# Optimization experiments

Measured on AMD Instinct MI355X. Metric: run time of the kernel, lower is better.

## Reference

```python
import jax, jax.numpy as jnp
import numpy as np
import math

N_USER = 100000
N_GAME = 50000
E = 200000
D = 256          # in_dim == out_dim
H = 8            # num_heads
SCALE = math.sqrt(D // H)  # sqrt(head_dim) = sqrt(32)


def setup_inputs() -> dict:
    key = jax.random.key(0)
    keys = jax.random.split(key, 64)
    it = iter(range(64))
    def nk():
        return keys[next(it)]
    s = 1.0 / math.sqrt(D)
    inp = {}
    inp["x_user"] = jax.random.normal(nk(), (N_USER, D), dtype=jnp.float32)
    inp["x_game"] = jax.random.normal(nk(), (N_GAME, D), dtype=jnp.float32)
    # node-type projections (k/q/v/out) for user and game
    for nt in ("user", "game"):
        for p in ("k", "q", "v", "out"):
            inp[f"W{p}_{nt}"] = jax.random.normal(nk(), (D, D), dtype=jnp.float32) * s
            inp[f"b{p}_{nt}"] = jax.random.normal(nk(), (D,), dtype=jnp.float32) * 0.01
    # edge-type attention + message transforms
    for et in ("played", "rev"):
        inp[f"Wa_{et}"] = jax.random.normal(nk(), (D, H), dtype=jnp.float32) * s
        inp[f"ba_{et}"] = jax.random.normal(nk(), (H,), dtype=jnp.float32) * 0.01
        inp[f"Wm_{et}"] = jax.random.normal(nk(), (D, D), dtype=jnp.float32) * s
        inp[f"bm_{et}"] = jax.random.normal(nk(), (D,), dtype=jnp.float32) * 0.01
    # edge indices: played (user -> game), rev_played (game -> user)
    inp["ei_played_src"] = jax.random.randint(nk(), (E,), 0, N_USER, dtype=jnp.int32)
    inp["ei_played_dst"] = jax.random.randint(nk(), (E,), 0, N_GAME, dtype=jnp.int32)
    inp["ei_rev_src"] = jax.random.randint(nk(), (E,), 0, N_GAME, dtype=jnp.int32)
    inp["ei_rev_dst"] = jax.random.randint(nk(), (E,), 0, N_USER, dtype=jnp.int32)
    return inp


def _lin(x, W, b):
    return x @ W + b


def _edge_pass(k_src_all, q_dst_all, v_src_all, Wa, ba, Wm, bm, src, dst, n_dst):
    # gather per-edge K/Q/V                                   [E, D]
    k_src = k_src_all[src]
    q_dst = q_dst_all[dst]
    v_src = v_src_all[src]
    # attention score MLP over head dim                       [E, H]
    scores = ((k_src * q_dst) @ Wa + ba) / SCALE
    attn = jax.nn.softmax(scores, axis=-1)  # softmax over heads (as in source)
    # message MLP                                             [E, D]
    msgs = v_src @ Wm + bm
    weighted = msgs * attn.mean(axis=-1, keepdims=True)
    # scatter-add to destination nodes
    agg = jax.ops.segment_sum(weighted, dst, num_segments=n_dst)
    cnt = jax.ops.segment_sum(jnp.ones((dst.shape[0], 1), weighted.dtype), dst, num_segments=n_dst)
    return agg, cnt


def reference(x_user, x_game,
              Wk_user, bk_user, Wq_user, bq_user, Wv_user, bv_user, Wout_user, bout_user,
              Wk_game, bk_game, Wq_game, bq_game, Wv_game, bv_game, Wout_game, bout_game,
              Wa_played, ba_played, Wm_played, bm_played,
              Wa_rev, ba_rev, Wm_rev, bm_rev,
              ei_played_src, ei_played_dst, ei_rev_src, ei_rev_dst):
    # per-node-type K/Q/V projections
    k_u = _lin(x_user, Wk_user, bk_user)
    q_u = _lin(x_user, Wq_user, bq_user)
    v_u = _lin(x_user, Wv_user, bv_user)
    k_g = _lin(x_game, Wk_game, bk_game)
    q_g = _lin(x_game, Wq_game, bq_game)
    v_g = _lin(x_game, Wv_game, bv_game)

    # user --played--> game
    agg_game, cnt_game = _edge_pass(k_u, q_g, v_u, Wa_played, ba_played, Wm_played, bm_played,
                                    ei_played_src, ei_played_dst, N_GAME)
    # game --rev_played--> user
    agg_user, cnt_user = _edge_pass(k_g, q_u, v_g, Wa_rev, ba_rev, Wm_rev, bm_rev,
                                    ei_rev_src, ei_rev_dst, N_USER)

    def finish(agg, cnt, x, Wout, bout):
        normed = agg / jnp.maximum(cnt, 1.0)
        return jax.nn.relu(_lin(normed, Wout, bout) + x)

    out_user = finish(agg_user, cnt_user, x_user, Wout_user, bout_user)
    out_game = finish(agg_game, cnt_game, x_game, Wout_game, bout_game)
    # concatenate node types for a single output array [N_USER+N_GAME, D]
    return jnp.concatenate([out_user, out_game], axis=0)
```

## Files before the change

kernel.cpp:

```cpp
#include <hip/hip_runtime.h>
#include <cstddef>
#include <cstdint>


#define DD 256
#define SCAN_CHUNK 2048

typedef __attribute__((ext_vector_type(8))) short short8;
typedef __attribute__((ext_vector_type(4))) float floatx4;

__device__ __forceinline__ short f2bf(float f) {
    union { float f; unsigned u; } c;
    c.f = f;
    unsigned r = c.u + 0x7fffu + ((c.u >> 16) & 1u);
    return (short)(r >> 16);
}

__device__ __forceinline__ float bflo(unsigned u) {
    union { unsigned u; float f; } c;
    c.u = u << 16;
    return c.f;
}
__device__ __forceinline__ float bfhi(unsigned u) {
    union { unsigned u; float f; } c;
    c.u = u & 0xffff0000u;
    return c.f;
}

__global__ __launch_bounds__(256) void fuseA(const float* __restrict__ A0,
                                             const float* __restrict__ B0,
                                             float* __restrict__ C0,
                                             const float* __restrict__ A1,
                                             const float* __restrict__ B1,
                                             float* __restrict__ C1,
                                             const int* __restrict__ dst0,
                                             int* __restrict__ cnt0, int E0,
                                             const int* __restrict__ dst1,
                                             int* __restrict__ cnt1, int E1) {
    __shared__ float As[DD];
    const int bid = blockIdx.x;
    const int c = threadIdx.x;
    if (bid < 512) {
        const int which = bid >> 8;
        const int r = bid & 255;
        const float* A = which ? A1 : A0;
        const float* B = which ? B1 : B0;
        float* C = which ? C1 : C0;
        As[c] = A[r * DD + c];
        __syncthreads();
        float acc = 0.f;
#pragma unroll 8
        for (int k = 0; k < DD; ++k) acc += As[k] * B[k * DD + c];
        C[r * DD + c] = acc;
    } else {
        const int nb0 = (E0 + 255) >> 8;
        const int b = bid - 512;
        if (b < nb0) {
            const int i = b * 256 + c;
            if (i < E0) atomicAdd(&cnt0[dst0[i]], 1);
        } else {
            const int i = (b - nb0) * 256 + c;
            if (i < E1) atomicAdd(&cnt1[dst1[i]], 1);
        }
    }
}

__global__ __launch_bounds__(256) void fuseB(const float* __restrict__ A0,
                                             const float* __restrict__ B0,
                                             short* __restrict__ C0,
                                             const float* __restrict__ A1,
                                             const float* __restrict__ B1,
                                             short* __restrict__ C1,
                                             int* __restrict__ off_g,
                                             int* __restrict__ sums_g, int n_g,
                                             int* __restrict__ off_u,
                                             int* __restrict__ sums_u, int n_u) {
    __shared__ float As[DD];
    __shared__ int ls[256];
    const int bid = blockIdx.x;
    const int tid = threadIdx.x;
    if (bid < 512) {
        const int which = bid >> 8;
        const int r = bid & 255;
        const int c = tid;
        const float* A = which ? A1 : A0;
        const float* B = which ? B1 : B0;
        short* C = which ? C1 : C0;
        As[c] = A[r * DD + c];
        __syncthreads();
        float acc = 0.f;
#pragma unroll 8
        for (int k = 0; k < DD; ++k) acc += As[k] * B[k * DD + c];
        const int idx = ((((r >> 5) * 16 + (c >> 4)) * 64 +
                          ((c & 15) | (((r >> 3) & 3) << 4))) << 3) + (r & 7);
        C[idx] = f2bf(acc * 0.125f);
    } else {
        const int nch_g = (n_g + SCAN_CHUNK - 1) / SCAN_CHUNK;
        const int b = bid - 512;
        int* off;
        int* sums;
        int n, cb;
        if (b < nch_g) { off = off_g; sums = sums_g; n = n_g; cb = b; }
        else { off = off_u; sums = sums_u; n = n_u; cb = b - nch_g; }
        const int base = cb * SCAN_CHUNK + tid * 8;
        int v[8];
        int s = 0;
#pragma unroll
        for (int i = 0; i < 8; ++i) {
            const int idx = base + i;
            v[i] = (idx < n) ? off[idx] : 0;
            s += v[i];
        }
        ls[tid] = s;
        __syncthreads();
        for (int d = 1; d < 256; d <<= 1) {
            const int t = (tid >= d) ? ls[tid - d] : 0;
            __syncthreads();
            ls[tid] += t;
            __syncthreads();
        }
        int excl = tid ? ls[tid - 1] : 0;
        if (tid == 255) sums[cb] = ls[255];
#pragma unroll
        for (int i = 0; i < 8; ++i) {
            const int idx = base + i;
            if (idx < n) off[idx] = excl;
            excl += v[i];
        }
    }
}

__global__ __launch_bounds__(256) void fuseC(const float* __restrict__ bv0,
                                             const float* __restrict__ Wm0,
                                             const float* __restrict__ bm0,
                                             const float* __restrict__ Wout0,
                                             float* __restrict__ bb0,
                                             const float* __restrict__ bv1,
                                             const float* __restrict__ Wm1,
                                             const float* __restrict__ bm1,
                                             const float* __restrict__ Wout1,
                                             float* __restrict__ bb1,
                                             int* __restrict__ sums_g, int nch_g,
                                             int* __restrict__ sums_u, int nch_u) {
    __shared__ float t[DD];
    __shared__ int ls[256];
    const int tid = threadIdx.x;
    if (blockIdx.x < 2) {
        const int w = blockIdx.x;
        const float* bv = w ? bv1 : bv0;
        const float* Wm = w ? Wm1 : Wm0;
        const float* bm = w ? bm1 : bm0;
        const float* Wout = w ? Wout1 : Wout0;
        float* bb = w ? bb1 : bb0;
        float acc = bm[tid];
#pragma unroll 8
        for (int k = 0; k < DD; ++k) acc += bv[k] * Wm[k * DD + tid];
        t[tid] = acc;
        __syncthreads();
        float acc2 = 0.f;
#pragma unroll 8
        for (int k = 0; k < DD; ++k) acc2 += t[k] * Wout[k * DD + tid];
        bb[tid] = acc2 * 0.125f;
    } else {
        int* sums = (blockIdx.x == 2) ? sums_g : sums_u;
        const int nch = (blockIdx.x == 2) ? nch_g : nch_u;
        ls[tid] = (tid < nch) ? sums[tid] : 0;
        __syncthreads();
        for (int d = 1; d < 256; d <<= 1) {
            const int t2 = (tid >= d) ? ls[tid - d] : 0;
            __syncthreads();
            ls[tid] += t2;
            __syncthreads();
        }
        if (tid < nch) sums[tid] = tid ? ls[tid - 1] : 0;
    }
}

__global__ __launch_bounds__(256) void fuseD(int* __restrict__ off_g,
                                             const int* __restrict__ sums_g,
                                             int* __restrict__ cur_g, int n_g, int Eg,
                                             int* __restrict__ off_u,
                                             const int* __restrict__ sums_u,
                                             int* __restrict__ cur_u, int n_u, int Eu) {
    const int gidx = blockIdx.x * 256 + threadIdx.x;
    const int span_g = n_g + 1;
    if (gidx < span_g) {
        if (gidx < n_g) {
            const int v = off_g[gidx] + sums_g[gidx / SCAN_CHUNK];
            off_g[gidx] = v;
            cur_g[gidx] = v;
        } else {
            off_g[n_g] = Eg;
        }
    } else {
        const int idx = gidx - span_g;
        if (idx < n_u) {
            const int v = off_u[idx] + sums_u[idx / SCAN_CHUNK];
            off_u[idx] = v;
            cur_u[idx] = v;
        } else if (idx == n_u) {
            off_u[n_u] = Eu;
        }
    }
}

__global__ __launch_bounds__(256, 4) void fuseE(
    const int* __restrict__ src0, const int* __restrict__ dst0,
    int* __restrict__ cur0, int* __restrict__ perm0, int E0,
    const int* __restrict__ src1, const int* __restrict__ dst1,
    int* __restrict__ cur1, int* __restrict__ perm1, int E1,
    const float* __restrict__ x_user, const float* __restrict__ x_game,
    const short* __restrict__ Bswp, const short* __restrict__ Bswr,
    short* __restrict__ Yp, short* __restrict__ Yr,
    int n_user, int n_game, int nyb_u, int nyb_g) {
    __shared__ short As[32][264];
    const int bid = blockIdx.x;
    const int tid = threadIdx.x;
    const int nyb = nyb_u + nyb_g;
    if (bid < nyb) {
        const int wave = __builtin_amdgcn_readfirstlane(tid >> 6);
        const int lane = tid & 63;
        const float* X;
        short* Y;
        const short* Bsw;
        int M, r0;
        if (bid < nyb_u) { X = x_user; Y = Yp; Bsw = Bswp; M = n_user; r0 = bid * 32; }
        else { X = x_game; Y = Yr; Bsw = Bswr; M = n_game; r0 = (bid - nyb_u) * 32; }

#pragma unroll
        for (int j = 0; j < 8; ++j) {
            const int lr = wave * 8 + j;
            const int r = r0 + lr;
            short4 b4 = {0, 0, 0, 0};
            if (r < M) {
                const float4 v = ((const float4*)(X + (size_t)r * DD))[lane];
                b4.x = f2bf(v.x);
                b4.y = f2bf(v.y);
                b4.z = f2bf(v.z);
                b4.w = f2bf(v.w);
            }
            *(short4*)&As[lr][lane * 4] = b4;
        }
        __syncthreads();

        const int quad = lane >> 4;
        const int l16 = lane & 15;
        floatx4 cacc[2][4];
#pragma unroll
        for (int rt = 0; rt < 2; ++rt)
#pragma unroll
            for (int ct = 0; ct < 4; ++ct) cacc[rt][ct] = (floatx4){0.f, 0.f, 0.f, 0.f};

        for (int kb8 = 0; kb8 < 8; ++kb8) {
            short8 af[2];
#pragma unroll
            for (int rt = 0; rt < 2; ++rt)
                af[rt] = *(const short8*)&As[rt * 16 + l16][kb8 * 32 + quad * 8];
            short8 bf[4];
            const short* bp = Bsw + (((size_t)(kb8 * 16 + wave * 4) * 64 + lane) << 3);
#pragma unroll
            for (int ct = 0; ct < 4; ++ct)
                bf[ct] = *(const short8*)(bp + (ct << 9));
#pragma unroll
            for (int rt = 0; rt < 2; ++rt)
#pragma unroll
                for (int ct = 0; ct < 4; ++ct)
                    cacc[rt][ct] = __builtin_amdgcn_mfma_f32_16x16x32_bf16(
                        af[rt], bf[ct], cacc[rt][ct], 0, 0, 0);
        }
        __syncthreads();

#pragma unroll
        for (int rt = 0; rt < 2; ++rt)
#pragma unroll
            for (int ct = 0; ct < 4; ++ct)
#pragma unroll
                for (int j = 0; j < 4; ++j)
                    As[rt * 16 + quad * 4 + j][wave * 64 + ct * 16 + l16] =
                        f2bf(cacc[rt][ct][j]);
        __syncthreads();
#pragma unroll
        for (int j = 0; j < 8; ++j) {
            const int lr = wave * 8 + j;
            const int r = r0 + lr;
            if (r < M)
                *(short4*)(Y + (size_t)r * DD + lane * 4) =
                    *(const short4*)&As[lr][lane * 4];
        }
    } else {
        const int b = bid - nyb;
        const int nb0 = (E0 + 255) >> 8;
        if (b < nb0) {
            const int i = b * 256 + tid;
            if (i < E0) {
                const int pos = atomicAdd(&cur0[dst0[i]], 1);
                perm0[pos] = src0[i];
            }
        } else {
            const int i = (b - nb0) * 256 + tid;
            if (i < E1) {
                const int pos = atomicAdd(&cur1[dst1[i]], 1);
                perm1[pos] = src1[i];
            }
        }
    }
}

__global__ __launch_bounds__(256, 4) void agg_relu(
    const short* __restrict__ Yp, const short* __restrict__ Yr,
    const int* __restrict__ perm_rev, const int* __restrict__ off_user,
    const float* __restrict__ bb_rev, const float* __restrict__ bout_user,
    const int* __restrict__ perm_played, const int* __restrict__ off_game,
    const float* __restrict__ bb_played, const float* __restrict__ bout_game,
    const float* __restrict__ x_user, const float* __restrict__ x_game,
    float* __restrict__ outp, int n_user, int n_game, int nb_game) {
    const int tid = threadIdx.x;
    const int wave = __builtin_amdgcn_readfirstlane(tid >> 6);
    const int lane = tid & 63;
    const int n0 = lane * 4;

    const short* Y;
    const int* perm;
    const int* off;
    const float* bb;
    const float* bout;
    const float* x_res;
    float* out;
    int M, r0;
    if ((int)blockIdx.x < nb_game) {
        Y = Yp;
        perm = perm_played;
        off = off_game;
        bb = bb_played;
        bout = bout_game;
        x_res = x_game;
        out = outp + (size_t)n_user * DD;
        M = n_game;
        r0 = (int)blockIdx.x * 32;
    } else {
        Y = Yr;
        perm = perm_rev;
        off = off_user;
        bb = bb_rev;
        bout = bout_user;
        x_res = x_user;
        out = outp;
        M = n_user;
        r0 = ((int)blockIdx.x - nb_game) * 32;
    }

    int e[8], en[8], deg[8];
    float4 acc[8];
#pragma unroll
    for (int j = 0; j < 8; ++j) {
        const int r = r0 + wave * 8 + j;
        e[j] = (r < M) ? off[r] : 0;
        en[j] = (r < M) ? off[r + 1] : 0;
        deg[j] = en[j] - e[j];
        acc[j].x = 0.f;
        acc[j].y = 0.f;
        acc[j].z = 0.f;
        acc[j].w = 0.f;
    }
    int mdeg = 0;
#pragma unroll
    for (int j = 0; j < 8; ++j) mdeg = max(mdeg, deg[j]);

    for (int t = 0; t < mdeg; ++t) {
        uint2 d[8];
        bool h[8];
#pragma unroll
        for (int j = 0; j < 8; ++j) {
            h[j] = e[j] < en[j];
            if (h[j]) {
                const int s = perm[e[j]++];
                d[j] = *(const uint2*)(Y + (size_t)s * DD + n0);
            }
        }
#pragma unroll
        for (int j = 0; j < 8; ++j) {
            if (h[j]) {
                acc[j].x += bflo(d[j].x);
                acc[j].y += bfhi(d[j].x);
                acc[j].z += bflo(d[j].y);
                acc[j].w += bfhi(d[j].y);
            }
        }
    }

    const float4 bbv = *(const float4*)(bb + n0);
    const float4 bov = *(const float4*)(bout + n0);
#pragma unroll
    for (int j = 0; j < 8; ++j) {
        const int r = r0 + wave * 8 + j;
        if (r < M) {
            const float inv = 1.0f / fmaxf((float)deg[j], 1.0f);
            const float beta = (deg[j] > 0) ? 1.0f : 0.0f;
            const float4 xr = *(const float4*)(x_res + (size_t)r * DD + n0);
            float4 o;
            o.x = fmaxf(acc[j].x * inv + beta * bbv.x + bov.x + xr.x, 0.f);
            o.y = fmaxf(acc[j].y * inv + beta * bbv.y + bov.y + xr.y, 0.f);
            o.z = fmaxf(acc[j].z * inv + beta * bbv.z + bov.z + xr.z, 0.f);
            o.w = fmaxf(acc[j].w * inv + beta * bbv.w + bov.w + xr.w, 0.f);
            *(float4*)(out + (size_t)r * DD + n0) = o;
        }
    }
}

extern "C" void kernel_launch(void* const* d_in, const int* in_sizes, int n_in,
                              void* d_out, int out_size, void* d_ws, size_t ws_size,
                              hipStream_t stream) {
    const float* x_user = (const float*)d_in[0];
    const float* x_game = (const float*)d_in[1];
    const float* Wv_user = (const float*)d_in[6];
    const float* bv_user = (const float*)d_in[7];
    const float* Wout_user = (const float*)d_in[8];
    const float* bout_user = (const float*)d_in[9];
    const float* Wv_game = (const float*)d_in[14];
    const float* bv_game = (const float*)d_in[15];
    const float* Wout_game = (const float*)d_in[16];
    const float* bout_game = (const float*)d_in[17];
    const float* Wm_played = (const float*)d_in[20];
    const float* bm_played = (const float*)d_in[21];
    const float* Wm_rev = (const float*)d_in[24];
    const float* bm_rev = (const float*)d_in[25];
    const int* ei_played_src = (const int*)d_in[26];
    const int* ei_played_dst = (const int*)d_in[27];
    const int* ei_rev_src = (const int*)d_in[28];
    const int* ei_rev_dst = (const int*)d_in[29];

    const int n_user = in_sizes[0] / DD;
    const int n_game = in_sizes[1] / DD;
    const int e_played = in_sizes[26];
    const int e_rev = in_sizes[28];

    float* out = (float*)d_out;

    float* fws = (float*)d_ws;
    float* T0 = fws;
    float* T1 = T0 + DD * DD;
    float* bb_played = T1 + DD * DD;
    float* bb_rev = bb_played + DD;
    short* Bsw_played = (short*)(bb_rev + DD);
    short* Bsw_rev = Bsw_played + DD * DD;
    int* iws = (int*)(Bsw_rev + DD * DD);
    int* off_game = iws;
    int* off_user = off_game + (n_game + 1);
    int* cursor_game = off_user + (n_user + 1);
    int* cursor_user = cursor_game + n_game;
    int* sums_game = cursor_user + n_user;
    int* sums_user = sums_game + 256;
    int* perm_played = sums_user + 256;
    int* perm_rev = perm_played + e_played;
    uintptr_t yaddr = (uintptr_t)(perm_rev + e_rev);
    yaddr = (yaddr + 255) & ~(uintptr_t)255;
    short* Yp = (short*)yaddr;
    short* Yr = Yp + (size_t)n_user * DD;
    (void)ws_size; (void)n_in; (void)out_size;

    hipMemsetAsync(off_game, 0, (size_t)(n_game + n_user + 2) * sizeof(int), stream);

    const int nbh_p = (e_played + 255) / 256;
    const int nbh_r = (e_rev + 255) / 256;
    const int nch_g = (n_game + SCAN_CHUNK - 1) / SCAN_CHUNK;
    const int nch_u = (n_user + SCAN_CHUNK - 1) / SCAN_CHUNK;

    fuseA<<<512 + nbh_p + nbh_r, 256, 0, stream>>>(
        Wv_user, Wm_played, T0, Wv_game, Wm_rev, T1,
        ei_played_dst, off_game, e_played, ei_rev_dst, off_user, e_rev);
    fuseB<<<512 + nch_g + nch_u, 256, 0, stream>>>(
        T0, Wout_game, Bsw_played, T1, Wout_user, Bsw_rev,
        off_game, sums_game, n_game, off_user, sums_user, n_user);
    fuseC<<<4, 256, 0, stream>>>(
        bv_user, Wm_played, bm_played, Wout_game, bb_played,
        bv_game, Wm_rev, bm_rev, Wout_user, bb_rev,
        sums_game, nch_g, sums_user, nch_u);
    const int ntot = (n_game + 1) + (n_user + 1);
    fuseD<<<(ntot + 255) / 256, 256, 0, stream>>>(
        off_game, sums_game, cursor_game, n_game, e_played,
        off_user, sums_user, cursor_user, n_user, e_rev);
    const int nyb_u = (n_user + 31) / 32;
    const int nyb_g = (n_game + 31) / 32;
    fuseE<<<nyb_u + nyb_g + nbh_p + nbh_r, 256, 0, stream>>>(
        ei_played_src, ei_played_dst, cursor_game, perm_played, e_played,
        ei_rev_src, ei_rev_dst, cursor_user, perm_rev, e_rev,
        x_user, x_game, Bsw_played, Bsw_rev, Yp, Yr,
        n_user, n_game, nyb_u, nyb_g);

    const int nb_game = (n_game + 31) / 32;
    const int nb_user = (n_user + 31) / 32;
    agg_relu<<<nb_game + nb_user, 256, 0, stream>>>(
        Yp, Yr, perm_rev, off_user, bb_rev, bout_user,
        perm_played, off_game, bb_played, bout_game,
        x_user, x_game, out, n_user, n_game, nb_game);
}
```

Baseline: 486.6 us.

## Merge all stages into one persistent kernel with global barriers

Replaces six kernel launches with a single persistent kernel of 1024 blocks that moves between stages through atomic-counter grid barriers. The bf16 MFMA projection tiles are split across barrier phases so they run alongside the scan, cursor and permutation work, hiding the small serial stages. This removes launch gaps and tail effects, but the grid barriers need every block resident at once (deadlock risk otherwise), and the fixed split points ya/yb are tuned by hand.

```diff
diff --git a/kernel.cpp b/kernel.cpp
--- a/kernel.cpp
+++ b/kernel.cpp
@@ -5,6 +5,8 @@
 
 #define DD 256
 #define SCAN_CHUNK 2048
+#define NB 1024
+#define NT 256
 
 typedef __attribute__((ext_vector_type(8))) short short8;
 typedef __attribute__((ext_vector_type(4))) float floatx4;
@@ -15,7 +17,6 @@
     unsigned r = c.u + 0x7fffu + ((c.u >> 16) & 1u);
     return (short)(r >> 16);
 }
-
 __device__ __forceinline__ float bflo(unsigned u) {
     union { unsigned u; float f; } c;
     c.u = u << 16;
@@ -27,295 +28,106 @@
     return c.f;
 }
 
-__global__ __launch_bounds__(256) void fuseA(const float* __restrict__ A0,
-                                             const float* __restrict__ B0,
-                                             float* __restrict__ C0,
-                                             const float* __restrict__ A1,
-                                             const float* __restrict__ B1,
-                                             float* __restrict__ C1,
-                                             const int* __restrict__ dst0,
-                                             int* __restrict__ cnt0, int E0,
-                                             const int* __restrict__ dst1,
-                                             int* __restrict__ cnt1, int E1) {
-    __shared__ float As[DD];
-    const int bid = blockIdx.x;
-    const int c = threadIdx.x;
-    if (bid < 512) {
-        const int which = bid >> 8;
-        const int r = bid & 255;
-        const float* A = which ? A1 : A0;
-        const float* B = which ? B1 : B0;
-        float* C = which ? C1 : C0;
-        As[c] = A[r * DD + c];
-        __syncthreads();
-        float acc = 0.f;
-#pragma unroll 8
-        for (int k = 0; k < DD; ++k) acc += As[k] * B[k * DD + c];
-        C[r * DD + c] = acc;
-    } else {
-        const int nb0 = (E0 + 255) >> 8;
-        const int b = bid - 512;
-        if (b < nb0) {
-            const int i = b * 256 + c;
-            if (i < E0) atomicAdd(&cnt0[dst0[i]], 1);
-        } else {
-            const int i = (b - nb0) * 256 + c;
-            if (i < E1) atomicAdd(&cnt1[dst1[i]], 1);
-        }
-    }
-}
-
-__global__ __launch_bounds__(256) void fuseB(const float* __restrict__ A0,
-                                             const float* __restrict__ B0,
-                                             short* __restrict__ C0,
-                                             const float* __restrict__ A1,
-                                             const float* __restrict__ B1,
-                                             short* __restrict__ C1,
-                                             int* __restrict__ off_g,
-                                             int* __restrict__ sums_g, int n_g,
-                                             int* __restrict__ off_u,
-                                             int* __restrict__ sums_u, int n_u) {
-    __shared__ float As[DD];
-    __shared__ int ls[256];
-    const int bid = blockIdx.x;
+__device__ __forceinline__ void gbar(int* bar, int target) {
+    __syncthreads();
+    if (threadIdx.x == 0) {
+        __threadfence();
+        __hip_atomic_fetch_add(bar, 1, __ATOMIC_ACQ_REL, __HIP_MEMORY_SCOPE_AGENT);
+        while (__hip_atomic_load(bar, __ATOMIC_ACQUIRE, __HIP_MEMORY_SCOPE_AGENT) < target)
+            __builtin_amdgcn_s_sleep(8);
+        __threadfence();
+    }
+    __syncthreads();
+}
+
+__device__ void ytile(int t, char* smem_,
+                      const float* __restrict__ x_user, const float* __restrict__ x_game,
+                      const short* __restrict__ Bswp, const short* __restrict__ Bswr,
+                      short* __restrict__ Yp, short* __restrict__ Yr,
+                      int n_user, int n_game, int nyb_u) {
+    short (*As)[264] = (short(*)[264])smem_;
     const int tid = threadIdx.x;
-    if (bid < 512) {
-        const int which = bid >> 8;
-        const int r = bid & 255;
-        const int c = tid;
-        const float* A = which ? A1 : A0;
-        const float* B = which ? B1 : B0;
-        short* C = which ? C1 : C0;
-        As[c] = A[r * DD + c];
-        __syncthreads();
-        float acc = 0.f;
-#pragma unroll 8
-        for (int k = 0; k < DD; ++k) acc += As[k] * B[k * DD + c];
-        const int idx = ((((r >> 5) * 16 + (c >> 4)) * 64 +
-                          ((c & 15) | (((r >> 3) & 3) << 4))) << 3) + (r & 7);
-        C[idx] = f2bf(acc * 0.125f);
-    } else {
-        const int nch_g = (n_g + SCAN_CHUNK - 1) / SCAN_CHUNK;
-        const int b = bid - 512;
-        int* off;
-        int* sums;
-        int n, cb;
-        if (b < nch_g) { off = off_g; sums = sums_g; n = n_g; cb = b; }
-        else { off = off_u; sums = sums_u; n = n_u; cb = b - nch_g; }
-        const int base = cb * SCAN_CHUNK + tid * 8;
-        int v[8];
-        int s = 0;
-#pragma unroll
-        for (int i = 0; i < 8; ++i) {
-            const int idx = base + i;
-            v[i] = (idx < n) ? off[idx] : 0;
-            s += v[i];
-        }
-        ls[tid] = s;
-        __syncthreads();
-        for (int d = 1; d < 256; d <<= 1) {
-            const int t = (tid >= d) ? ls[tid - d] : 0;
-            __syncthreads();
-            ls[tid] += t;
-            __syncthreads();
-        }
-        int excl = tid ? ls[tid - 1] : 0;
-        if (tid == 255) sums[cb] = ls[255];
-#pragma unroll
-        for (int i = 0; i < 8; ++i) {
-            const int idx = base + i;
-            if (idx < n) off[idx] = excl;
-            excl += v[i];
-        }
-    }
-}
-
-__global__ __launch_bounds__(256) void fuseC(const float* __restrict__ bv0,
-                                             const float* __restrict__ Wm0,
-                                             const float* __restrict__ bm0,
-                                             const float* __restrict__ Wout0,
-                                             float* __restrict__ bb0,
-                                             const float* __restrict__ bv1,
-                                             const float* __restrict__ Wm1,
-                                             const float* __restrict__ bm1,
-                                             const float* __restrict__ Wout1,
-                                             float* __restrict__ bb1,
-                                             int* __restrict__ sums_g, int nch_g,
-                                             int* __restrict__ sums_u, int nch_u) {
-    __shared__ float t[DD];
-    __shared__ int ls[256];
+    const int wave = tid >> 6;
+    const int lane = tid & 63;
+    const float* X;
+    short* Y;
+    const short* Bsw;
+    int M, r0;
+    if (t < nyb_u) { X = x_user; Y = Yp; Bsw = Bswp; M = n_user; r0 = t * 32; }
+    else { X = x_game; Y = Yr; Bsw = Bswr; M = n_game; r0 = (t - nyb_u) * 32; }
+
+#pragma unroll
+    for (int j = 0; j < 8; ++j) {
+        const int lr = wave * 8 + j;
+        const int r = r0 + lr;
+        short4 b4 = {0, 0, 0, 0};
+        if (r < M) {
+            const float4 v = ((const float4*)(X + (size_t)r * DD))[lane];
+            b4.x = f2bf(v.x);
+            b4.y = f2bf(v.y);
+            b4.z = f2bf(v.z);
+            b4.w = f2bf(v.w);
+        }
+        *(short4*)&As[lr][lane * 4] = b4;
+    }
+    __syncthreads();
+
+    const int quad = lane >> 4;
+    const int l16 = lane & 15;
+    floatx4 cacc[2][4];
+#pragma unroll
+    for (int rt = 0; rt < 2; ++rt)
+#pragma unroll
+        for (int ct = 0; ct < 4; ++ct) cacc[rt][ct] = (floatx4){0.f, 0.f, 0.f, 0.f};
+
+    for (int kb8 = 0; kb8 < 8; ++kb8) {
+        short8 af[2];
+#pragma unroll
+        for (int rt = 0; rt < 2; ++rt)
+            af[rt] = *(const short8*)&As[rt * 16 + l16][kb8 * 32 + quad * 8];
+        short8 bf[4];
+        const short* bp = Bsw + (((size_t)(kb8 * 16 + wave * 4) * 64 + lane) << 3);
+#pragma unroll
+        for (int ct = 0; ct < 4; ++ct)
+            bf[ct] = *(const short8*)(bp + (ct << 9));
+#pragma unroll
+        for (int rt = 0; rt < 2; ++rt)
+#pragma unroll
+            for (int ct = 0; ct < 4; ++ct)
+                cacc[rt][ct] = __builtin_amdgcn_mfma_f32_16x16x32_bf16(
+                    af[rt], bf[ct], cacc[rt][ct], 0, 0, 0);
+    }
+    __syncthreads();
+
+#pragma unroll
+    for (int rt = 0; rt < 2; ++rt)
+#pragma unroll
+        for (int ct = 0; ct < 4; ++ct)
+#pragma unroll
+            for (int j = 0; j < 4; ++j)
+                As[rt * 16 + quad * 4 + j][wave * 64 + ct * 16 + l16] =
+                    f2bf(cacc[rt][ct][j]);
+    __syncthreads();
+#pragma unroll
+    for (int j = 0; j < 8; ++j) {
+        const int lr = wave * 8 + j;
+        const int r = r0 + lr;
+        if (r < M)
+            *(short4*)(Y + (size_t)r * DD + lane * 4) = *(const short4*)&As[lr][lane * 4];
+    }
+    __syncthreads();
+}
+
+__device__ void aggtile(int t,
+                        const short* __restrict__ Yp, const short* __restrict__ Yr,
+                        const int* __restrict__ perm_rev, const int* __restrict__ off_user,
+                        const float* __restrict__ bb_rev, const float* __restrict__ bout_user,
+                        const int* __restrict__ perm_played, const int* __restrict__ off_game,
+                        const float* __restrict__ bb_played, const float* __restrict__ bout_game,
+                        const float* __restrict__ x_user, const float* __restrict__ x_game,
+                        float* __restrict__ outp, int n_user, int n_game, int nbt_g) {
     const int tid = threadIdx.x;
-    if (blockIdx.x < 2) {
-        const int w = blockIdx.x;
-        const float* bv = w ? bv1 : bv0;
-        const float* Wm = w ? Wm1 : Wm0;
-        const float* bm = w ? bm1 : bm0;
-        const float* Wout = w ? Wout1 : Wout0;
-        float* bb = w ? bb1 : bb0;
-        float acc = bm[tid];
-#pragma unroll 8
-        for (int k = 0; k < DD; ++k) acc += bv[k] * Wm[k * DD + tid];
-        t[tid] = acc;
-        __syncthreads();
-        float acc2 = 0.f;
-#pragma unroll 8
-        for (int k = 0; k < DD; ++k) acc2 += t[k] * Wout[k * DD + tid];
-        bb[tid] = acc2 * 0.125f;
-    } else {
-        int* sums = (blockIdx.x == 2) ? sums_g : sums_u;
-        const int nch = (blockIdx.x == 2) ? nch_g : nch_u;
-        ls[tid] = (tid < nch) ? sums[tid] : 0;
-        __syncthreads();
-        for (int d = 1; d < 256; d <<= 1) {
-            const int t2 = (tid >= d) ? ls[tid - d] : 0;
-            __syncthreads();
-            ls[tid] += t2;
-            __syncthreads();
-        }
-        if (tid < nch) sums[tid] = tid ? ls[tid - 1] : 0;
-    }
-}
-
-__global__ __launch_bounds__(256) void fuseD(int* __restrict__ off_g,
-                                             const int* __restrict__ sums_g,
-                                             int* __restrict__ cur_g, int n_g, int Eg,
-                                             int* __restrict__ off_u,
-                                             const int* __restrict__ sums_u,
-                                             int* __restrict__ cur_u, int n_u, int Eu) {
-    const int gidx = blockIdx.x * 256 + threadIdx.x;
-    const int span_g = n_g + 1;
-    if (gidx < span_g) {
-        if (gidx < n_g) {
-            const int v = off_g[gidx] + sums_g[gidx / SCAN_CHUNK];
-            off_g[gidx] = v;
-            cur_g[gidx] = v;
-        } else {
-            off_g[n_g] = Eg;
-        }
-    } else {
-        const int idx = gidx - span_g;
-        if (idx < n_u) {
-            const int v = off_u[idx] + sums_u[idx / SCAN_CHUNK];
-            off_u[idx] = v;
-            cur_u[idx] = v;
-        } else if (idx == n_u) {
-            off_u[n_u] = Eu;
-        }
-    }
-}
-
-__global__ __launch_bounds__(256, 4) void fuseE(
-    const int* __restrict__ src0, const int* __restrict__ dst0,
-    int* __restrict__ cur0, int* __restrict__ perm0, int E0,
-    const int* __restrict__ src1, const int* __restrict__ dst1,
-    int* __restrict__ cur1, int* __restrict__ perm1, int E1,
-    const float* __restrict__ x_user, const float* __restrict__ x_game,
-    const short* __restrict__ Bswp, const short* __restrict__ Bswr,
-    short* __restrict__ Yp, short* __restrict__ Yr,
-    int n_user, int n_game, int nyb_u, int nyb_g) {
-    __shared__ short As[32][264];
-    const int bid = blockIdx.x;
-    const int tid = threadIdx.x;
-    const int nyb = nyb_u + nyb_g;
-    if (bid < nyb) {
-        const int wave = __builtin_amdgcn_readfirstlane(tid >> 6);
-        const int lane = tid & 63;
-        const float* X;
-        short* Y;
-        const short* Bsw;
-        int M, r0;
-        if (bid < nyb_u) { X = x_user; Y = Yp; Bsw = Bswp; M = n_user; r0 = bid * 32; }
-        else { X = x_game; Y = Yr; Bsw = Bswr; M = n_game; r0 = (bid - nyb_u) * 32; }
-
-#pragma unroll
-        for (int j = 0; j < 8; ++j) {
-            const int lr = wave * 8 + j;
-            const int r = r0 + lr;
-            short4 b4 = {0, 0, 0, 0};
-            if (r < M) {
-                const float4 v = ((const float4*)(X + (size_t)r * DD))[lane];
-                b4.x = f2bf(v.x);
-                b4.y = f2bf(v.y);
-                b4.z = f2bf(v.z);
-                b4.w = f2bf(v.w);
-            }
-            *(short4*)&As[lr][lane * 4] = b4;
-        }
-        __syncthreads();
-
-        const int quad = lane >> 4;
-        const int l16 = lane & 15;
-        floatx4 cacc[2][4];
-#pragma unroll
-        for (int rt = 0; rt < 2; ++rt)
-#pragma unroll
-            for (int ct = 0; ct < 4; ++ct) cacc[rt][ct] = (floatx4){0.f, 0.f, 0.f, 0.f};
-
-        for (int kb8 = 0; kb8 < 8; ++kb8) {
-            short8 af[2];
-#pragma unroll
-            for (int rt = 0; rt < 2; ++rt)
-                af[rt] = *(const short8*)&As[rt * 16 + l16][kb8 * 32 + quad * 8];
-            short8 bf[4];
-            const short* bp = Bsw + (((size_t)(kb8 * 16 + wave * 4) * 64 + lane) << 3);
-#pragma unroll
-            for (int ct = 0; ct < 4; ++ct)
-                bf[ct] = *(const short8*)(bp + (ct << 9));
-#pragma unroll
-            for (int rt = 0; rt < 2; ++rt)
-#pragma unroll
-                for (int ct = 0; ct < 4; ++ct)
-                    cacc[rt][ct] = __builtin_amdgcn_mfma_f32_16x16x32_bf16(
-                        af[rt], bf[ct], cacc[rt][ct], 0, 0, 0);
-        }
-        __syncthreads();
-
-#pragma unroll
-        for (int rt = 0; rt < 2; ++rt)
-#pragma unroll
-            for (int ct = 0; ct < 4; ++ct)
-#pragma unroll
-                for (int j = 0; j < 4; ++j)
-                    As[rt * 16 + quad * 4 + j][wave * 64 + ct * 16 + l16] =
-                        f2bf(cacc[rt][ct][j]);
-        __syncthreads();
-#pragma unroll
-        for (int j = 0; j < 8; ++j) {
-            const int lr = wave * 8 + j;
-            const int r = r0 + lr;
-            if (r < M)
-                *(short4*)(Y + (size_t)r * DD + lane * 4) =
-                    *(const short4*)&As[lr][lane * 4];
-        }
-    } else {
-        const int b = bid - nyb;
-        const int nb0 = (E0 + 255) >> 8;
-        if (b < nb0) {
-            const int i = b * 256 + tid;
-            if (i < E0) {
-                const int pos = atomicAdd(&cur0[dst0[i]], 1);
-                perm0[pos] = src0[i];
-            }
-        } else {
-            const int i = (b - nb0) * 256 + tid;
-            if (i < E1) {
-                const int pos = atomicAdd(&cur1[dst1[i]], 1);
-                perm1[pos] = src1[i];
-            }
-        }
-    }
-}
-
-__global__ __launch_bounds__(256, 4) void agg_relu(
-    const short* __restrict__ Yp, const short* __restrict__ Yr,
-    const int* __restrict__ perm_rev, const int* __restrict__ off_user,
-    const float* __restrict__ bb_rev, const float* __restrict__ bout_user,
-    const int* __restrict__ perm_played, const int* __restrict__ off_game,
-    const float* __restrict__ bb_played, const float* __restrict__ bout_game,
-    const float* __restrict__ x_user, const float* __restrict__ x_game,
-    float* __restrict__ outp, int n_user, int n_game, int nb_game) {
-    const int tid = threadIdx.x;
-    const int wave = __builtin_amdgcn_readfirstlane(tid >> 6);
+    const int wave = tid >> 6;
     const int lane = tid & 63;
     const int n0 = lane * 4;
 
@@ -327,26 +139,12 @@
     const float* x_res;
     float* out;
     int M, r0;
-    if ((int)blockIdx.x < nb_game) {
-        Y = Yp;
-        perm = perm_played;
-        off = off_game;
-        bb = bb_played;
-        bout = bout_game;
-        x_res = x_game;
-        out = outp + (size_t)n_user * DD;
-        M = n_game;
-        r0 = (int)blockIdx.x * 32;
+    if (t < nbt_g) {
+        Y = Yp; perm = perm_played; off = off_game; bb = bb_played; bout = bout_game;
+        x_res = x_game; out = outp + (size_t)n_user * DD; M = n_game; r0 = t * 32;
     } else {
-        Y = Yr;
-        perm = perm_rev;
-        off = off_user;
-        bb = bb_rev;
-        bout = bout_user;
-        x_res = x_user;
-        out = outp;
-        M = n_user;
-        r0 = ((int)blockIdx.x - nb_game) * 32;
+        Y = Yr; perm = perm_rev; off = off_user; bb = bb_rev; bout = bout_user;
+        x_res = x_user; out = outp; M = n_user; r0 = (t - nbt_g) * 32;
     }
 
     int e[8], en[8], deg[8];
@@ -357,16 +155,13 @@
         e[j] = (r < M) ? off[r] : 0;
         en[j] = (r < M) ? off[r + 1] : 0;
         deg[j] = en[j] - e[j];
-        acc[j].x = 0.f;
-        acc[j].y = 0.f;
-        acc[j].z = 0.f;
-        acc[j].w = 0.f;
+        acc[j].x = 0.f; acc[j].y = 0.f; acc[j].z = 0.f; acc[j].w = 0.f;
     }
     int mdeg = 0;
 #pragma unroll
     for (int j = 0; j < 8; ++j) mdeg = max(mdeg, deg[j]);
 
-    for (int t = 0; t < mdeg; ++t) {
+    for (int it = 0; it < mdeg; ++it) {
         uint2 d[8];
         bool h[8];
 #pragma unroll
@@ -405,6 +200,205 @@
             *(float4*)(out + (size_t)r * DD + n0) = o;
         }
     }
+}
+
+__global__ __launch_bounds__(256, 4) void mega(
+    const float* __restrict__ x_user, const float* __restrict__ x_game,
+    const float* __restrict__ Wv_user, const float* __restrict__ bv_user,
+    const float* __restrict__ Wout_user, const float* __restrict__ bout_user,
+    const float* __restrict__ Wv_game, const float* __restrict__ bv_game,
+    const float* __restrict__ Wout_game, const float* __restrict__ bout_game,
+    const float* __restrict__ Wm_played, const float* __restrict__ bm_played,
+    const float* __restrict__ Wm_rev, const float* __restrict__ bm_rev,
+    const int* __restrict__ eps, const int* __restrict__ epd,
+    const int* __restrict__ ers, const int* __restrict__ erd,
+    int n_user, int n_game, int e_played, int e_rev,
+    float* __restrict__ T0, float* __restrict__ T1,
+    float* __restrict__ tv0, float* __restrict__ tv1,
+    float* __restrict__ bb_played, float* __restrict__ bb_rev,
+    short* __restrict__ Bsw_played, short* __restrict__ Bsw_rev,
+    int* __restrict__ bar,
+    int* __restrict__ off_game, int* __restrict__ off_user,
+    int* __restrict__ cursor_game, int* __restrict__ cursor_user,
+    int* __restrict__ sums_game, int* __restrict__ sums_user,
+    int* __restrict__ perm_played, int* __restrict__ perm_rev,
+    short* __restrict__ Yp, short* __restrict__ Yr,
+    float* __restrict__ outp,
+    int nbh_p, int nbh_r, int nch_g, int nch_u,
+    int nyb_u, int nyb_g, int ya, int yb) {
+    __shared__ __align__(16) char smem[32 * 264 * 2];
+    float* fsm = (float*)smem;
+    int* ism = (int*)smem;
+    const int bid = blockIdx.x;
+    const int tid = threadIdx.x;
+    const int ytot = nyb_u + nyb_g;
+
+    if (bid < 512) {
+        const int which = bid >> 8;
+        const int r = bid & 255;
+        const float* A = which ? Wv_game : Wv_user;
+        const float* B = which ? Wm_rev : Wm_played;
+        float* C = which ? T1 : T0;
+        fsm[tid] = A[r * DD + tid];
+        __syncthreads();
+        float acc = 0.f;
+#pragma unroll 8
+        for (int k = 0; k < DD; ++k) acc += fsm[k] * B[k * DD + tid];
+        C[r * DD + tid] = acc;
+    } else if (bid < 514) {
+        const int w = bid - 512;
+        const float* bv = w ? bv_game : bv_user;
+        const float* Wm = w ? Wm_rev : Wm_played;
+        const float* bm = w ? bm_rev : bm_played;
+        float* tv = w ? tv1 : tv0;
+        float acc = bm[tid];
+#pragma unroll 8
+        for (int k = 0; k < DD; ++k) acc += bv[k] * Wm[k * DD + tid];
+        tv[tid] = acc;
+    } else {
+        for (int t = bid - 514; t < nbh_p + nbh_r; t += NB - 514) {
+            if (t < nbh_p) {
+                const int i = t * NT + tid;
+                if (i < e_played) atomicAdd(&off_game[epd[i]], 1);
+            } else {
+                const int i = (t - nbh_p) * NT + tid;
+                if (i < e_rev) atomicAdd(&off_user[erd[i]], 1);
+            }
+        }
+    }
+    gbar(bar, NB);
+
+    if (bid < 512) {
+        const int which = bid >> 8;
+        const int r = bid & 255;
+        const float* A = which ? T1 : T0;
+        const float* B = which ? Wout_user : Wout_game;
+        short* C = which ? Bsw_rev : Bsw_played;
+        fsm[tid] = A[r * DD + tid];
+        __syncthreads();
+        float acc = 0.f;
+#pragma unroll 8
+        for (int k = 0; k < DD; ++k) acc += fsm[k] * B[k * DD + tid];
+        const int idx = ((((r >> 5) * 16 + (tid >> 4)) * 64 +
+                          ((tid & 15) | (((r >> 3) & 3) << 4))) << 3) + (r & 7);
+        C[idx] = f2bf(acc * 0.125f);
+    } else if (bid < 514) {
+        const int w = bid - 512;
+        const float* tsrc = w ? tv1 : tv0;
+        const float* Wo = w ? Wout_user : Wout_game;
+        float* bb = w ? bb_rev : bb_played;
+        float acc = 0.f;
+#pragma unroll 8
+        for (int k = 0; k < DD; ++k) acc += tsrc[k] * Wo[k * DD + tid];
+        bb[tid] = acc * 0.125f;
+    } else if (bid - 514 < nch_g + nch_u) {
+        const int t = bid - 514;
+        int* off;
+        int* sums;
+        int n, cb;
+        if (t < nch_g) { off = off_game; sums = sums_game; n = n_game; cb = t; }
+        else { off = off_user; sums = sums_user; n = n_user; cb = t - nch_g; }
+        const int base = cb * SCAN_CHUNK + tid * 8;
+        int v[8];
+        int s = 0;
+#pragma unroll
+        for (int i = 0; i < 8; ++i) {
+            const int idx = base + i;
+            v[i] = (idx < n) ? off[idx] : 0;
+            s += v[i];
+        }
+        ism[tid] = s;
+        __syncthreads();
+        for (int d = 1; d < 256; d <<= 1) {
+            const int t2 = (tid >= d) ? ism[tid - d] : 0;
+            __syncthreads();
+            ism[tid] += t2;
+            __syncthreads();
+        }
+        int excl = tid ? ism[tid - 1] : 0;
+        if (tid == 255) sums[cb] = ism[255];
+#pragma unroll
+        for (int i = 0; i < 8; ++i) {
+            const int idx = base + i;
+            if (idx < n) off[idx] = excl;
+            excl += v[i];
+        }
+    }
+    gbar(bar, 2 * NB);
+
+    if (bid < 2) {
+        int* sums = bid ? sums_user : sums_game;
+        const int nch = bid ? nch_u : nch_g;
+        ism[tid] = (tid < nch) ? sums[tid] : 0;
+        __syncthreads();
+        for (int d = 1; d < 256; d <<= 1) {
+            const int t2 = (tid >= d) ? ism[tid - d] : 0;
+            __syncthreads();
+            ism[tid] += t2;
+            __syncthreads();
+        }
+        if (tid < nch) sums[tid] = tid ? ism[tid - 1] : 0;
+        __syncthreads();
+    }
+    for (int t = bid; t < ya; t += NB)
+        ytile(t, smem, x_user, x_game, Bsw_played, Bsw_rev, Yp, Yr,
+              n_user, n_game, nyb_u);
+    gbar(bar, 3 * NB);
+
+    {
+        const int gidx = bid * NT + tid;
+        const int span_g = n_game + 1;
+        const int ntot = span_g + n_user + 1;
+        if (gidx < ntot) {
+            if (gidx < span_g) {
+                if (gidx < n_game) {
+                    const int v = off_game[gidx] + sums_game[gidx / SCAN_CHUNK];
+                    off_game[gidx] = v;
+                    cursor_game[gidx] = v;
+                } else {
+                    off_game[n_game] = e_played;
+                }
+            } else {
+                const int idx = gidx - span_g;
+                if (idx < n_user) {
+                    const int v = off_user[idx] + sums_user[idx / SCAN_CHUNK];
+                    off_user[idx] = v;
+                    cursor_user[idx] = v;
+                } else {
+                    off_user[n_user] = e_rev;
+                }
+            }
+        }
+    }
+    for (int t = ya + bid; t < yb; t += NB)
+        ytile(t, smem, x_user, x_game, Bsw_played, Bsw_rev, Yp, Yr,
+              n_user, n_game, nyb_u);
+    gbar(bar, 4 * NB);
+
+    for (int t = bid; t < nbh_p + nbh_r; t += NB) {
+        if (t < nbh_p) {
+            const int i = t * NT + tid;
+            if (i < e_played) {
+                const int pos = atomicAdd(&cursor_game[epd[i]], 1);
+                perm_played[pos] = eps[i];
+            }
+        } else {
+            const int i = (t - nbh_p) * NT + tid;
+            if (i < e_rev) {
+                const int pos = atomicAdd(&cursor_user[erd[i]], 1);
+                perm_rev[pos] = ers[i];
+            }
+        }
+    }
+    for (int t = yb + bid; t < ytot; t += NB)
+        ytile(t, smem, x_user, x_game, Bsw_played, Bsw_rev, Yp, Yr,
+              n_user, n_game, nyb_u);
+    gbar(bar, 5 * NB);
+
+    for (int t = bid; t < nyb_g + nyb_u; t += NB)
+        aggtile(t, Yp, Yr, perm_rev, off_user, bb_rev, bout_user,
+                perm_played, off_game, bb_played, bout_game,
+                x_user, x_game, outp, n_user, n_game, nyb_g);
 }
 
 extern "C" void kernel_launch(void* const* d_in, const int* in_sizes, int n_in,
@@ -441,10 +435,13 @@
     float* T1 = T0 + DD * DD;
     float* bb_played = T1 + DD * DD;
     float* bb_rev = bb_played + DD;
-    short* Bsw_played = (short*)(bb_rev + DD);
+    float* tv0 = bb_rev + DD;
+    float* tv1 = tv0 + DD;
+    short* Bsw_played = (short*)(tv1 + DD);
     short* Bsw_rev = Bsw_played + DD * DD;
     int* iws = (int*)(Bsw_rev + DD * DD);
-    int* off_game = iws;
+    int* bar = iws;
+    int* off_game = bar + 8;
     int* off_user = off_game + (n_game + 1);
     int* cursor_game = off_user + (n_user + 1);
     int* cursor_user = cursor_game + n_game;
@@ -458,39 +455,31 @@
     short* Yr = Yp + (size_t)n_user * DD;
     (void)ws_size; (void)n_in; (void)out_size;
 
-    hipMemsetAsync(off_game, 0, (size_t)(n_game + n_user + 2) * sizeof(int), stream);
-
     const int nbh_p = (e_played + 255) / 256;
     const int nbh_r = (e_rev + 255) / 256;
     const int nch_g = (n_game + SCAN_CHUNK - 1) / SCAN_CHUNK;
     const int nch_u = (n_user + SCAN_CHUNK - 1) / SCAN_CHUNK;
-
-    fuseA<<<512 + nbh_p + nbh_r, 256, 0, stream>>>(
-        Wv_user, Wm_played, T0, Wv_game, Wm_rev, T1,
-        ei_played_dst, off_game, e_played, ei_rev_dst, off_user, e_rev);
-    fuseB<<<512 + nch_g + nch_u, 256, 0, stream>>>(
-        T0, Wout_game, Bsw_played, T1, Wout_user, Bsw_rev,
-        off_game, sums_game, n_game, off_user, sums_user, n_user);
-    fuseC<<<4, 256, 0, stream>>>(
-        bv_user, Wm_played, bm_played, Wout_game, bb_played,
-        bv_game, Wm_rev, bm_rev, Wout_user, bb_rev,
-        sums_game, nch_g, sums_user, nch_u);
-    const int ntot = (n_game + 1) + (n_user + 1);
-    fuseD<<<(ntot + 255) / 256, 256, 0, stream>>>(
-        off_game, sums_game, cursor_game, n_game, e_played,
-        off_user, sums_user, cursor_user, n_user, e_rev);
     const int nyb_u = (n_user + 31) / 32;
     const int nyb_g = (n_game + 31) / 32;
-    fuseE<<<nyb_u + nyb_g + nbh_p + nbh_r, 256, 0, stream>>>(
-        ei_played_src, ei_played_dst, cursor_game, perm_played, e_played,
-        ei_rev_src, ei_rev_dst, cursor_user, perm_rev, e_rev,
-        x_user, x_game, Bsw_played, Bsw_rev, Yp, Yr,
-        n_user, n_game, nyb_u, nyb_g);
-
-    const int nb_game = (n_game + 31) / 32;
-    const int nb_user = (n_user + 31) / 32;
-    agg_relu<<<nb_game + nb_user, 256, 0, stream>>>(
-        Yp, Yr, perm_rev, off_user, bb_rev, bout_user,
-        perm_played, off_game, bb_played, bout_game,
-        x_user, x_game, out, n_user, n_game, nb_game);
-}
+    const int ytot = nyb_u + nyb_g;
+    int ya = 1900; if (ya > ytot) ya = ytot;
+    int yb = 3400; if (yb > ytot) yb = ytot;
+    if (yb < ya) yb = ya;
+
+    hipMemsetAsync(bar, 0, (size_t)(8 + (n_game + 1) + (n_user + 1)) * sizeof(int),
+                   stream);
+
+    mega<<<NB, NT, 0, stream>>>(
+        x_user, x_game,
+        Wv_user, bv_user, Wout_user, bout_user,
+        Wv_game, bv_game, Wout_game, bout_game,
+        Wm_played, bm_played, Wm_rev, bm_rev,
+        ei_played_src, ei_played_dst, ei_rev_src, ei_rev_dst,
+        n_user, n_game, e_played, e_rev,
+        T0, T1, tv0, tv1, bb_played, bb_rev,
+        Bsw_played, Bsw_rev,
+        bar, off_game, off_user, cursor_game, cursor_user,
+        sums_game, sums_user, perm_played, perm_rev,
+        Yp, Yr, out,
+        nbh_p, nbh_r, nch_g, nch_u, nyb_u, nyb_g, ya, yb);
+}
```

New measurement: 1.652 ms. +239.4%, slower.
